# Performance work log

Hardware: AMD Instinct MI355X
Metric: run time of the kernel (lower is better)

The kernel has to match this reference:

```python
import jax, jax.numpy as jnp
import numpy as np
from jax import lax

T_DATA = 20000
E_NO = 2000
I_NO = 500
SUB_NO = 16
SYN_B = 3
HID = 256
T_SYN = 200
T_ENC = 80


def _causal_conv(x, kern):
    # x: [T, S] per-subunit drive; kern: [S, K] causal kernels (index = lag)
    S, K = kern.shape
    lhs = jnp.pad(x.T, ((0, 0), (K - 1, 0)))[None]        # [1, S, T+K-1]
    rhs = kern[:, ::-1][:, None, :]                        # flip then correlate == torch conv1d path
    out = lax.conv_general_dilated(lhs, rhs, (1,), 'VALID', feature_group_count=S)
    return out[0].T                                        # [T, S]


def setup_inputs() -> dict:
    key = jax.random.key(0)
    ks = jax.random.split(key, 16)
    V_in = jax.random.normal(ks[0], (T_DATA,), jnp.float32) * 5.0 - 69.0
    S_e = jax.random.bernoulli(ks[1], 0.02, (T_DATA, E_NO)).astype(jnp.float32)
    S_i = jax.random.bernoulli(ks[2], 0.02, (T_DATA, I_NO)).astype(jnp.float32)
    # synapse -> subunit one-hot assignment matrices [sub_no, n_syn]
    C_syn_e = jax.nn.one_hot(jax.random.randint(ks[3], (E_NO,), 0, SUB_NO), SUB_NO, dtype=jnp.float32).T
    C_syn_i = jax.nn.one_hot(jax.random.randint(ks[4], (I_NO,), 0, SUB_NO), SUB_NO, dtype=jnp.float32).T
    # parameters, initialized exactly as in __init__
    K_syn = jnp.stack([jnp.full((SUB_NO, SYN_B), 0.04),
                       jnp.full((SUB_NO, SYN_B), -0.02),
                       jnp.full((SUB_NO, SYN_B), 0.02)], axis=-1)          # [sub, B, 3]
    tau_syn = jnp.tile((jnp.arange(SYN_B, dtype=jnp.float32) + 1.6)[:, None], (1, 3))  # [B, 3]
    delta_syn = jnp.full((SUB_NO, 2), 2.0, jnp.float32)
    enc_bias = jnp.zeros((SUB_NO - 1,), jnp.float32)
    W_in = 2 * T_ENC - 1

    def lin(k, fan_out, fan_in):
        kw, kb = jax.random.split(k)
        s = 1.0 / np.sqrt(fan_in)
        return (jax.random.uniform(kw, (fan_out, fan_in), jnp.float32, -s, s),
                jax.random.uniform(kb, (fan_out,), jnp.float32, -s, s))

    W1, b1 = lin(ks[5], HID, W_in)
    W2, b2 = lin(ks[6], HID, HID)
    W3, b3 = lin(ks[7], HID, HID)
    W4, b4 = lin(ks[8], SUB_NO - 1, HID)
    a1 = jnp.float32(0.25)
    a2 = jnp.float32(0.25)
    a3 = jnp.float32(0.25)
    return dict(V_in=V_in, S_e=S_e, S_i=S_i, C_syn_e=C_syn_e, C_syn_i=C_syn_i,
                K_syn=K_syn, tau_syn=tau_syn, delta_syn=delta_syn, enc_bias=enc_bias,
                W1=W1, b1=b1, a1=a1, W2=W2, b2=b2, a2=a2, W3=W3, b3=b3, a3=a3,
                W4=W4, b4=b4)


def reference(V_in, S_e, S_i, C_syn_e, C_syn_i, K_syn, tau_syn, delta_syn, enc_bias,
              W1, b1, a1, W2, b2, a2, W3, b3, a3, W4, b4):
    T = V_in.shape[0]
    # ---- spike_convolve, fully vectorized over (subunit, basis) ----
    t = jnp.arange(T_SYN, dtype=V_in.dtype)                 # [T_syn]
    d = jnp.exp(delta_syn)                                   # [sub, 2]
    te = jnp.maximum(t[None, :] - d[:, 0:1], 0.0)            # [sub, T_syn]
    ti = jnp.maximum(t[None, :] - d[:, 1:2], 0.0)
    tau = jnp.exp(tau_syn)                                   # [B, 3]
    tte = te[:, None, :] / tau[None, :, 0, None]             # [sub, B, T_syn]
    tti = ti[:, None, :] / tau[None, :, 1, None]
    ker_e = jnp.einsum('sbt,sb->st', tte * jnp.exp(-tte), K_syn[:, :, 0])
    ker_i = jnp.einsum('sbt,sb->st', tti * jnp.exp(-tti), K_syn[:, :, 1])
    in_e = S_e @ C_syn_e.T                                   # [T, sub]
    in_i = S_i @ C_syn_i.T
    S_conv = _causal_conv(in_e, ker_e) + _causal_conv(in_i, ker_i)   # [T, sub]
    # ---- encode: batched sliding-window MLP (replaces per-timestep loop) ----
    W = 2 * T_ENC - 1
    Vpad = jnp.zeros((T + W,), V_in.dtype).at[T_ENC - 1:T_ENC - 1 + T].set(V_in)
    idx = jnp.arange(T)[:, None] + jnp.arange(W)[None, :]    # [T, W]
    win = Vpad[idx]                                          # [T, W]
    prelu = lambda x, a: jnp.where(x >= 0, x, a * x)
    h = prelu(win @ W1.T + b1, a1)
    h = prelu(h @ W2.T + b2, a2)
    h = prelu(h @ W3.T + b3, a3)
    nn_out = h @ W4.T + b4                                   # [T, sub-1]
    return jax.nn.sigmoid(nn_out + S_conv[:, 1:] + enc_bias)
```

## Files before the change

kernel.cpp:

```cpp
#include <hip/hip_runtime.h>
#include <cstdint>
#include <cstddef>

#define T_DATA 20000
#define E_NO 2000
#define I_NO 500
#define SUB_NO 16
#define HID 256
#define T_SYN 200
#define T_ENC 80
#define W_IN 159

typedef __attribute__((ext_vector_type(8))) __bf16 bf16x8;
typedef __attribute__((ext_vector_type(8))) short short8;
typedef __attribute__((ext_vector_type(4))) float floatx4;
typedef __attribute__((ext_vector_type(4))) unsigned int uint4v;
typedef __attribute__((ext_vector_type(2))) unsigned int uint2v;

__device__ __forceinline__ float bf2f(unsigned short u) {
    union { unsigned int i; float f; } v; v.i = ((unsigned int)u) << 16; return v.f;
}
__device__ __forceinline__ unsigned short f2bf(float f) {
    union { float f; unsigned int i; } v; v.f = f;
    unsigned int r = v.i + 0x7FFFu + ((v.i >> 16) & 1u);
    return (unsigned short)(r >> 16);
}
__device__ __forceinline__ float inload(const void* p, int i, int isbf) {
    return isbf ? bf2f(((const unsigned short*)p)[i]) : ((const float*)p)[i];
}

__device__ __forceinline__ int detect_bf(const void* Se, int* sfl) {
    if (threadIdx.x == 0) *sfl = 0;
    __syncthreads();
    const unsigned int* w = (const unsigned int*)Se;
    int la = 0;
    #pragma unroll
    for (int i = 0; i < 4; i++)
        la |= (w[i * 256 + threadIdx.x] & 0xFFFFu) ? 1 : 0;
    if (la) atomicOr(sfl, 1);
    __syncthreads();
    return *sfl;
}

#define OFF_KERE   16u
#define OFF_KERI   12816u
#define OFF_W1H    25616u
#define OFF_W1L    107536u
#define OFF_W2H    189456u
#define OFF_W2L    320528u
#define OFF_W3H    451600u
#define OFF_W3L    582672u
#define OFF_W4H    713744u
#define OFF_W4L    721424u
#define OFF_INE    729104u
#define OFF_INI    1049104u

__device__ __forceinline__ void acc_slot(unsigned int b, unsigned int sh,
                                         unsigned long long& lo, unsigned long long& hi) {
    unsigned int up = sh >> 6;
    unsigned int s6 = sh & 63;
    lo += (unsigned long long)(b & (up ^ 1u)) << s6;
    hi += (unsigned long long)(b & up) << s6;
}

#define SPIKE_BLOCKS 1250
#define SETUP_ITEMS  182272
#define SETUP_BLOCKS 712

__global__ void __launch_bounds__(256) k_front(
        const void* Se, const void* Si, const void* Ce, const void* Ci,
        const void* Ksyn, const void* tau_syn, const void* dly,
        const void* W1, const void* W2, const void* W3, const void* W4,
        float* ker_e, float* ker_i,
        unsigned short* W1h, unsigned short* W1l,
        unsigned short* W2h, unsigned short* W2l,
        unsigned short* W3h, unsigned short* W3l,
        unsigned short* W4h, unsigned short* W4l,
        unsigned char* in_e, unsigned char* in_i) {
    __shared__ int sfl;
    __shared__ __align__(8) unsigned char she[E_NO];
    __shared__ __align__(8) unsigned char shi[I_NO];
    int tid = threadIdx.x;

    if (blockIdx.x < SPIKE_BLOCKS) {
        if (tid == 0) sfl = 0;
        __syncthreads();
        {
            const unsigned int* w = (const unsigned int*)Se;
            int la = 0;
            #pragma unroll
            for (int i = 0; i < 4; i++)
                la |= (w[i * 256 + tid] & 0xFFFFu) ? 1 : 0;
            if (la) atomicOr(&sfl, 1);
        }
        __syncthreads();
        int f = sfl;
        for (int e = tid; e < E_NO; e += 256) {
            int a = 0;
            for (int s = 0; s < 16; s++) if (inload(Ce, s * E_NO + e, f) > 0.5f) a = s;
            she[e] = (unsigned char)(a * 8);
        }
        for (int e = tid; e < I_NO; e += 256) {
            int a = 0;
            for (int s = 0; s < 16; s++) if (inload(Ci, s * I_NO + e, f) > 0.5f) a = s;
            shi[e] = (unsigned char)(a * 8);
        }
        __syncthreads();
        int lane = tid & 63, wave = tid >> 6;
        #pragma unroll
        for (int j = 0; j < 4; j++) {
            int t = blockIdx.x * 16 + wave * 4 + j;
            unsigned long long e0 = 0, e1 = 0, i0 = 0, i1 = 0;
            if (f) {
                const uint4v* re = (const uint4v*)((const unsigned short*)Se + (size_t)t * E_NO);
                #pragma unroll
                for (int it = 0; it < 4; it++) {
                    int c = it * 64 + lane;
                    if (c < 250) {
                        uint4v v = re[c];
                        unsigned long long q = *(const unsigned long long*)&she[c * 8];
                        #pragma unroll
                        for (int w = 0; w < 4; w++) {
                            unsigned int x = v[w];
                            acc_slot((x >> 7) & 1u,  (unsigned int)(q >> (16 * w)) & 0xFFu, e0, e1);
                            acc_slot((x >> 23) & 1u, (unsigned int)(q >> (16 * w + 8)) & 0xFFu, e0, e1);
                        }
                    }
                }
                const uint2v* ri = (const uint2v*)((const unsigned short*)Si + (size_t)t * I_NO);
                #pragma unroll
                for (int it = 0; it < 2; it++) {
                    int c = it * 64 + lane;
                    if (c < 125) {
                        uint2v v = ri[c];
                        unsigned int q = *(const unsigned int*)&shi[c * 4];
                        #pragma unroll
                        for (int w = 0; w < 2; w++) {
                            unsigned int x = v[w];
                            acc_slot((x >> 7) & 1u,  (q >> (16 * w)) & 0xFFu, i0, i1);
                            acc_slot((x >> 23) & 1u, (q >> (16 * w + 8)) & 0xFFu, i0, i1);
                        }
                    }
                }
            } else {
                const uint4v* re = (const uint4v*)((const float*)Se + (size_t)t * E_NO);
                #pragma unroll
                for (int it = 0; it < 8; it++) {
                    int c = it * 64 + lane;
                    if (c < 500) {
                        uint4v v = re[c];
                        unsigned int q = *(const unsigned int*)&she[c * 4];
                        #pragma unroll
                        for (int w = 0; w < 4; w++)
                            acc_slot((v[w] >> 23) & 1u, (q >> (8 * w)) & 0xFFu, e0, e1);
                    }
                }
                const uint2v* ri = (const uint2v*)((const float*)Si + (size_t)t * I_NO);
                #pragma unroll
                for (int it = 0; it < 4; it++) {
                    int c = it * 64 + lane;
                    if (c < 250) {
                        uint2v v = ri[c];
                        unsigned int q = *(const unsigned short*)&shi[c * 2];
                        #pragma unroll
                        for (int w = 0; w < 2; w++)
                            acc_slot((v[w] >> 23) & 1u, (q >> (8 * w)) & 0xFFu, i0, i1);
                    }
                }
            }
            for (int off = 32; off; off >>= 1) {
                e0 += __shfl_xor(e0, off);
                e1 += __shfl_xor(e1, off);
                i0 += __shfl_xor(i0, off);
                i1 += __shfl_xor(i1, off);
            }
            if (lane < 16) {
                unsigned long long a = (lane < 8) ? e0 : e1;
                in_e[(size_t)t * 16 + lane] = (unsigned char)((a >> ((lane & 7) * 8)) & 0xFF);
            } else if (lane < 32) {
                int s = lane - 16;
                unsigned long long a = (s < 8) ? i0 : i1;
                in_i[(size_t)t * 16 + s] = (unsigned char)((a >> ((s & 7) * 8)) & 0xFF);
            }
        }
    } else {
        int f = detect_bf(Se, &sfl);
        int id = (blockIdx.x - SPIKE_BLOCKS) * 256 + tid;
        if (id < 6400) {
            int c = id < 3200 ? 0 : 1;
            int q = id - c * 3200;
            int s = q / 200, j = q - s * 200;
            float d = expf(inload(dly, s * 2 + c, f));
            float tt = fmaxf((float)j - d, 0.0f);
            float acc = 0.f;
            #pragma unroll
            for (int b = 0; b < 3; b++) {
                float tau = expf(inload(tau_syn, b * 3 + c, f));
                float x = tt / tau;
                acc += x * expf(-x) * inload(Ksyn, (s * 3 + b) * 3 + c, f);
            }
            (c == 0 ? ker_e : ker_i)[s * 200 + j] = acc;
        } else if (id < 47360) {
            int q = id - 6400;
            int n = q / 160, k = q - n * 160;
            float v = (k < W_IN) ? inload(W1, n * W_IN + k, f) : 0.f;
            unsigned short hi = f2bf(v);
            W1h[q] = hi;
            W1l[q] = f2bf(v - bf2f(hi));
        } else if (id < 112896) {
            int q = id - 47360;
            float v = inload(W2, q, f);
            unsigned short hi = f2bf(v);
            W2h[q] = hi;
            W2l[q] = f2bf(v - bf2f(hi));
        } else if (id < 178432) {
            int q = id - 112896;
            float v = inload(W3, q, f);
            unsigned short hi = f2bf(v);
            W3h[q] = hi;
            W3l[q] = f2bf(v - bf2f(hi));
        } else if (id < 182272) {
            int q = id - 178432;
            float v = inload(W4, q, f);
            unsigned short hi = f2bf(v);
            W4h[q] = hi;
            W4l[q] = f2bf(v - bf2f(hi));
        }
    }
}

template<bool BF>
__device__ __forceinline__ void mlp_body(
    const void* V,
    const unsigned short* W1h, const unsigned short* W1l, const void* b1, const void* a1p,
    const unsigned short* W2h, const unsigned short* W2l, const void* b2, const void* a2p,
    const unsigned short* W3h, const unsigned short* W3l, const void* b3, const void* a3p,
    const unsigned short* W4h, const unsigned short* W4l, const void* b4,
    const void* encb, const float* sc, void* out,
    unsigned short* Ahi, unsigned short* Alo)
{
    int tid = threadIdx.x;
    int lane = tid & 63, wave = tid >> 6;
    int lm = lane & 15, quad = lane >> 4;
    int t0 = blockIdx.x * 64;

    auto ld = [&](const void* p, int i) -> float {
        return BF ? bf2f(((const unsigned short*)p)[i]) : ((const float*)p)[i];
    };

    for (int idx = tid; idx < 64 * 160; idx += 256) {
        int m = idx / 160, k = idx - m * 160;
        int tg = t0 + m + k - (T_ENC - 1);
        float v = 0.f;
        if (k < W_IN && tg >= 0 && tg < T_DATA) v = ld(V, tg);
        unsigned short hi = f2bf(v);
        int col = (((k >> 3) ^ (m & 31)) << 3) | (k & 7);
        Ahi[m * 256 + col] = hi;
        if (!BF) Alo[m * 256 + col] = f2bf(v - bf2f(hi));
    }
    __syncthreads();

    floatx4 acc[4][4];
    auto aoff = [&](int mt, int ks) {
        int arow = mt * 16 + lm;
        return arow * 256 + ((((ks << 2) | quad) ^ (arow & 31)) << 3);
    };

    auto epi = [&](const void* bias, float alpha) {
        __syncthreads();
        #pragma unroll
        for (int mt = 0; mt < 4; mt++) {
            #pragma unroll
            for (int nt = 0; nt < 4; nt++) {
                int cn = wave * 64 + nt * 16 + lm;
                float bb = ld(bias, cn);
                #pragma unroll
                for (int j = 0; j < 4; j++) {
                    int row = mt * 16 + quad * 4 + j;
                    float h = acc[mt][nt][j] + bb;
                    h = (h >= 0.f) ? h : alpha * h;
                    unsigned short hi = f2bf(h);
                    int col = (((cn >> 3) ^ (row & 31)) << 3) | (cn & 7);
                    Ahi[row * 256 + col] = hi;
                    if (!BF) Alo[row * 256 + col] = f2bf(h - bf2f(hi));
                }
            }
        }
        __syncthreads();
    };

    floatx4 z = {0.f, 0.f, 0.f, 0.f};
    {
        #pragma unroll
        for (int mt = 0; mt < 4; mt++)
            #pragma unroll
            for (int nt = 0; nt < 4; nt++) acc[mt][nt] = z;
        if (BF) {
            bf16x8 Bh[5][4];
            #pragma unroll
            for (int ks = 0; ks < 5; ks++)
                #pragma unroll
                for (int nt = 0; nt < 4; nt++)
                    Bh[ks][nt] = *(const bf16x8*)(W1h + (size_t)(wave * 64 + nt * 16 + lm) * 160 + ks * 32 + quad * 8);
            #pragma unroll
            for (int ks = 0; ks < 5; ks++) {
                bf16x8 a[4];
                #pragma unroll
                for (int mt = 0; mt < 4; mt++) a[mt] = *(const bf16x8*)&Ahi[aoff(mt, ks)];
                #pragma unroll
                for (int nt = 0; nt < 4; nt++)
                    #pragma unroll
                    for (int mt = 0; mt < 4; mt++)
                        acc[mt][nt] = __builtin_amdgcn_mfma_f32_16x16x32_bf16(a[mt], Bh[ks][nt], acc[mt][nt], 0, 0, 0);
            }
        } else {
            for (int ks = 0; ks < 5; ks++) {
                bf16x8 ah[4], al[4];
                #pragma unroll
                for (int mt = 0; mt < 4; mt++) {
                    ah[mt] = *(const bf16x8*)&Ahi[aoff(mt, ks)];
                    al[mt] = *(const bf16x8*)&Alo[aoff(mt, ks)];
                }
                #pragma unroll
                for (int nt = 0; nt < 4; nt++) {
                    size_t bo = (size_t)(wave * 64 + nt * 16 + lm) * 160 + ks * 32 + quad * 8;
                    bf16x8 bh = *(const bf16x8*)(W1h + bo);
                    bf16x8 bl = *(const bf16x8*)(W1l + bo);
                    #pragma unroll
                    for (int mt = 0; mt < 4; mt++) {
                        acc[mt][nt] = __builtin_amdgcn_mfma_f32_16x16x32_bf16(ah[mt], bh, acc[mt][nt], 0, 0, 0);
                        acc[mt][nt] = __builtin_amdgcn_mfma_f32_16x16x32_bf16(al[mt], bh, acc[mt][nt], 0, 0, 0);
                        acc[mt][nt] = __builtin_amdgcn_mfma_f32_16x16x32_bf16(ah[mt], bl, acc[mt][nt], 0, 0, 0);
                    }
                }
            }
        }
        epi(b1, ld(a1p, 0));
    }
    const unsigned short* Whs[2] = {W2h, W3h};
    const unsigned short* Wls[2] = {W2l, W3l};
    const void* bs[2] = {b2, b3};
    const void* as_[2] = {a2p, a3p};
    for (int l = 0; l < 2; l++) {
        #pragma unroll
        for (int mt = 0; mt < 4; mt++)
            #pragma unroll
            for (int nt = 0; nt < 4; nt++) acc[mt][nt] = z;
        const unsigned short* Wh = Whs[l];
        const unsigned short* Wl = Wls[l];
        if (BF) {
            bf16x8 Bh[8][4];
            #pragma unroll
            for (int ks = 0; ks < 8; ks++)
                #pragma unroll
                for (int nt = 0; nt < 4; nt++)
                    Bh[ks][nt] = *(const bf16x8*)(Wh + (size_t)(wave * 64 + nt * 16 + lm) * 256 + ks * 32 + quad * 8);
            #pragma unroll
            for (int ks = 0; ks < 8; ks++) {
                bf16x8 a[4];
                #pragma unroll
                for (int mt = 0; mt < 4; mt++) a[mt] = *(const bf16x8*)&Ahi[aoff(mt, ks)];
                #pragma unroll
                for (int nt = 0; nt < 4; nt++)
                    #pragma unroll
                    for (int mt = 0; mt < 4; mt++)
                        acc[mt][nt] = __builtin_amdgcn_mfma_f32_16x16x32_bf16(a[mt], Bh[ks][nt], acc[mt][nt], 0, 0, 0);
            }
        } else {
            for (int ks = 0; ks < 8; ks++) {
                bf16x8 ah[4], al[4];
                #pragma unroll
                for (int mt = 0; mt < 4; mt++) {
                    ah[mt] = *(const bf16x8*)&Ahi[aoff(mt, ks)];
                    al[mt] = *(const bf16x8*)&Alo[aoff(mt, ks)];
                }
                #pragma unroll
                for (int nt = 0; nt < 4; nt++) {
                    size_t bo = (size_t)(wave * 64 + nt * 16 + lm) * 256 + ks * 32 + quad * 8;
                    bf16x8 bh = *(const bf16x8*)(Wh + bo);
                    bf16x8 bl = *(const bf16x8*)(Wl + bo);
                    #pragma unroll
                    for (int mt = 0; mt < 4; mt++) {
                        acc[mt][nt] = __builtin_amdgcn_mfma_f32_16x16x32_bf16(ah[mt], bh, acc[mt][nt], 0, 0, 0);
                        acc[mt][nt] = __builtin_amdgcn_mfma_f32_16x16x32_bf16(al[mt], bh, acc[mt][nt], 0, 0, 0);
                        acc[mt][nt] = __builtin_amdgcn_mfma_f32_16x16x32_bf16(ah[mt], bl, acc[mt][nt], 0, 0, 0);
                    }
                }
            }
        }
        epi(bs[l], ld(as_[l], 0));
    }
    {
        int mt = wave;
        short8 z8 = {0, 0, 0, 0, 0, 0, 0, 0};
        bf16x8 bz = __builtin_bit_cast(bf16x8, z8);
        floatx4 a4 = z;
        #pragma unroll
        for (int ks = 0; ks < 8; ks++) {
            bf16x8 ah = *(const bf16x8*)&Ahi[aoff(mt, ks)];
            bf16x8 bh = bz;
            if (lm < 15)
                bh = *(const bf16x8*)(W4h + (size_t)lm * 256 + ks * 32 + quad * 8);
            a4 = __builtin_amdgcn_mfma_f32_16x16x32_bf16(ah, bh, a4, 0, 0, 0);
            if (!BF) {
                bf16x8 al = *(const bf16x8*)&Alo[aoff(mt, ks)];
                bf16x8 bl = bz;
                if (lm < 15)
                    bl = *(const bf16x8*)(W4l + (size_t)lm * 256 + ks * 32 + quad * 8);
                a4 = __builtin_amdgcn_mfma_f32_16x16x32_bf16(al, bh, a4, 0, 0, 0);
                a4 = __builtin_amdgcn_mfma_f32_16x16x32_bf16(ah, bl, a4, 0, 0, 0);
            }
        }
        if (lm < 15) {
            float bb = ld(b4, lm) + ld(encb, lm);
            #pragma unroll
            for (int j = 0; j < 4; j++) {
                int row = mt * 16 + quad * 4 + j;
                int t = t0 + row;
                if (t < T_DATA) {
                    float x = a4[j] + bb + sc[row * 16 + lm + 1];
                    x = fminf(fmaxf(x, -40.f), 40.f);
                    float sg = 1.f / (1.f + expf(-x));
                    if (BF) ((unsigned short*)out)[(size_t)t * 15 + lm] = f2bf(sg);
                    else    ((float*)out)[(size_t)t * 15 + lm] = sg;
                }
            }
        }
    }
}

__global__ void __launch_bounds__(256, 2) k_back(
    const void* Se, const void* V,
    const unsigned char* in_e, const unsigned char* in_i,
    const float* ker_e, const float* ker_i,
    const unsigned short* W1h, const unsigned short* W1l, const void* b1, const void* a1p,
    const unsigned short* W2h, const unsigned short* W2l, const void* b2, const void* a2p,
    const unsigned short* W3h, const unsigned short* W3l, const void* b3, const void* a3p,
    const unsigned short* W4h, const unsigned short* W4l, const void* b4,
    const void* encb, void* out) {
    __shared__ __align__(16) char smem[65536];
    __shared__ __align__(16) float sc[64 * 16];
    __shared__ int sfl;
    int f = detect_bf(Se, &sfl);
    int tid = threadIdx.x;
    int t0 = blockIdx.x * 64;

    {
        float* se = (float*)smem;
        float* si = se + 263 * 17;
        float* ke = si + 263 * 17;
        float* ki = ke + 16 * 201;
        for (int idx = tid; idx < 263 * 4; idx += 256) {
            int r = idx >> 2, wi = idx & 3;
            int t = t0 - 199 + r;
            unsigned int ve = 0, vi = 0;
            if (t >= 0 && t < T_DATA) {
                ve = ((const unsigned int*)in_e)[t * 4 + wi];
                vi = ((const unsigned int*)in_i)[t * 4 + wi];
            }
            #pragma unroll
            for (int b = 0; b < 4; b++) {
                se[r * 17 + wi * 4 + b] = (float)((ve >> (8 * b)) & 0xFF);
                si[r * 17 + wi * 4 + b] = (float)((vi >> (8 * b)) & 0xFF);
            }
        }
        for (int idx = tid; idx < 3200; idx += 256) {
            int s = idx / 200, j = idx - s * 200;
            ke[s * 201 + j] = ker_e[idx];
            ki[s * 201 + j] = ker_i[idx];
        }
        __syncthreads();
        int s = tid & 15, g4 = (tid >> 4) * 4;
        float a0 = 0.f, a1 = 0.f, a2 = 0.f, a3 = 0.f;
        float w0 = se[(g4 + 199) * 17 + s], w1 = se[(g4 + 200) * 17 + s];
        float w2 = se[(g4 + 201) * 17 + s], w3 = se[(g4 + 202) * 17 + s];
        float x0 = si[(g4 + 199) * 17 + s], x1 = si[(g4 + 200) * 17 + s];
        float x2 = si[(g4 + 201) * 17 + s], x3 = si[(g4 + 202) * 17 + s];
        #pragma unroll 4
        for (int j = 0; j < 200; j++) {
            float kej = ke[s * 201 + j];
            float kij = ki[s * 201 + j];
            a0 += w0 * kej + x0 * kij;
            a1 += w1 * kej + x1 * kij;
            a2 += w2 * kej + x2 * kij;
            a3 += w3 * kej + x3 * kij;
            int lr = g4 + 198 - j; lr = lr < 0 ? 0 : lr;
            float nw = se[lr * 17 + s], nx = si[lr * 17 + s];
            w3 = w2; w2 = w1; w1 = w0; w0 = nw;
            x3 = x2; x2 = x1; x1 = x0; x0 = nx;
        }
        sc[(g4 + 0) * 16 + s] = a0;
        sc[(g4 + 1) * 16 + s] = a1;
        sc[(g4 + 2) * 16 + s] = a2;
        sc[(g4 + 3) * 16 + s] = a3;
        __syncthreads();
    }

    unsigned short* Ahi = (unsigned short*)smem;
    unsigned short* Alo = Ahi + 64 * 256;
    if (f)
        mlp_body<true>(V, W1h, W1l, b1, a1p, W2h, W2l, b2, a2p, W3h, W3l, b3, a3p,
                       W4h, W4l, b4, encb, sc, out, Ahi, Alo);
    else
        mlp_body<false>(V, W1h, W1l, b1, a1p, W2h, W2l, b2, a2p, W3h, W3l, b3, a3p,
                        W4h, W4l, b4, encb, sc, out, Ahi, Alo);
}

extern "C" void kernel_launch(void* const* d_in, const int* in_sizes, int n_in,
                              void* d_out, int out_size, void* d_ws, size_t ws_size,
                              hipStream_t stream) {
    const void* V    = d_in[0];
    const void* Se   = d_in[1];
    const void* Si   = d_in[2];
    const void* Ce   = d_in[3];
    const void* Ci   = d_in[4];
    const void* Ksyn = d_in[5];
    const void* tau  = d_in[6];
    const void* dly  = d_in[7];
    const void* encb = d_in[8];
    const void* W1   = d_in[9];
    const void* b1   = d_in[10];
    const void* a1   = d_in[11];
    const void* W2   = d_in[12];
    const void* b2   = d_in[13];
    const void* a2   = d_in[14];
    const void* W3   = d_in[15];
    const void* b3   = d_in[16];
    const void* a3   = d_in[17];
    const void* W4   = d_in[18];
    const void* b4   = d_in[19];

    char* w = (char*)d_ws;
    float* ker_e = (float*)(w + OFF_KERE);
    float* ker_i = (float*)(w + OFF_KERI);
    unsigned short* W1h = (unsigned short*)(w + OFF_W1H);
    unsigned short* W1l = (unsigned short*)(w + OFF_W1L);
    unsigned short* W2h = (unsigned short*)(w + OFF_W2H);
    unsigned short* W2l = (unsigned short*)(w + OFF_W2L);
    unsigned short* W3h = (unsigned short*)(w + OFF_W3H);
    unsigned short* W3l = (unsigned short*)(w + OFF_W3L);
    unsigned short* W4h = (unsigned short*)(w + OFF_W4H);
    unsigned short* W4l = (unsigned short*)(w + OFF_W4L);
    unsigned char* in_e = (unsigned char*)(w + OFF_INE);
    unsigned char* in_i = (unsigned char*)(w + OFF_INI);

    k_front<<<SPIKE_BLOCKS + SETUP_BLOCKS, 256, 0, stream>>>(
        Se, Si, Ce, Ci, Ksyn, tau, dly, W1, W2, W3, W4,
        ker_e, ker_i, W1h, W1l, W2h, W2l, W3h, W3l, W4h, W4l, in_e, in_i);
    k_back<<<313, 256, 0, stream>>>(
        Se, V, in_e, in_i, ker_e, ker_i,
        W1h, W1l, b1, a1, W2h, W2l, b2, a2, W3h, W3l, b3, a3,
        W4h, W4l, b4, encb, d_out);
}
```

Before: 381.4 us.

## Compute spike-to-subunit projection with bf16 MFMA instead of bit-packed scalar accumulation

Replaces the per-timestep scalar bit-extraction and packed 64-bit counter accumulation for S_e@C_e^T and S_i@C_i^T with 16x16x32 bf16 MFMA instructions. The one-hot matrices are loaded directly as MFMA A fragments, so the per-block shared-memory assignment table is no longer built. Each wave covers a K slice, and the partial sums are reduced through shared memory and rounded to bytes. Float inputs are truncated to bf16, which is exact for 0/1 values. Format detection now runs in all blocks.

```diff
diff --git a/kernel.cpp b/kernel.cpp
--- a/kernel.cpp
+++ b/kernel.cpp
@@ -55,17 +55,102 @@
 #define OFF_INE    729104u
 #define OFF_INI    1049104u
 
-__device__ __forceinline__ void acc_slot(unsigned int b, unsigned int sh,
-                                         unsigned long long& lo, unsigned long long& hi) {
-    unsigned int up = sh >> 6;
-    unsigned int s6 = sh & 63;
-    lo += (unsigned long long)(b & (up ^ 1u)) << s6;
-    hi += (unsigned long long)(b & up) << s6;
-}
-
 #define SPIKE_BLOCKS 1250
-#define SETUP_ITEMS  182272
 #define SETUP_BLOCKS 712
+
+__device__ __forceinline__ bf16x8 hi_pack(uint4v u0, uint4v u1) {
+    uint4v r;
+    r[0] = (u0[0] >> 16) | (u0[1] & 0xFFFF0000u);
+    r[1] = (u0[2] >> 16) | (u0[3] & 0xFFFF0000u);
+    r[2] = (u1[0] >> 16) | (u1[1] & 0xFFFF0000u);
+    r[3] = (u1[2] >> 16) | (u1[3] & 0xFFFF0000u);
+    return __builtin_bit_cast(bf16x8, r);
+}
+template<bool BF>
+__device__ __forceinline__ bf16x8 ldfrag(const void* p, size_t idx) {
+    if (BF) return *(const bf16x8*)((const unsigned short*)p + idx);
+    const float* f = (const float*)p + idx;
+    return hi_pack(*(const uint4v*)f, *(const uint4v*)(f + 4));
+}
+template<bool BF>
+__device__ __forceinline__ bf16x8 ldfrag4(const void* p, size_t idx) {
+    uint4v r = {0u, 0u, 0u, 0u};
+    if (BF) {
+        uint2v u = *(const uint2v*)((const unsigned short*)p + idx);
+        r[0] = u[0]; r[1] = u[1];
+    } else {
+        uint4v u = *(const uint4v*)((const float*)p + idx);
+        r[0] = (u[0] >> 16) | (u[1] & 0xFFFF0000u);
+        r[1] = (u[2] >> 16) | (u[3] & 0xFFFF0000u);
+    }
+    return __builtin_bit_cast(bf16x8, r);
+}
+
+template<bool BF>
+__device__ __forceinline__ void spike_gemm(const void* Se, const void* Si,
+        const void* Ce, const void* Ci,
+        unsigned char* in_e, unsigned char* in_i, float* red) {
+    int tid = threadIdx.x;
+    int lane = tid & 63, wave = tid >> 6;
+    int lm = lane & 15, quad = lane >> 4;
+    int t0 = blockIdx.x * 16;
+    size_t teb = (size_t)(t0 + lm) * E_NO;
+    size_t tib = (size_t)(t0 + lm) * I_NO;
+    floatx4 ae = {0.f, 0.f, 0.f, 0.f}, ai = {0.f, 0.f, 0.f, 0.f};
+    short8 zs = {0, 0, 0, 0, 0, 0, 0, 0};
+    bf16x8 bz = __builtin_bit_cast(bf16x8, zs);
+
+    #pragma unroll
+    for (int q = 0; q < 16; q++) {
+        int kg = wave * 16 + q;
+        int k0 = kg * 32 + quad * 8;
+        bf16x8 a = bz, b = bz;
+        if (kg < 63 && (kg < 62 || quad < 2)) {
+            a = ldfrag<BF>(Ce, (size_t)lm * E_NO + k0);
+            b = ldfrag<BF>(Se, teb + k0);
+        }
+        ae = __builtin_amdgcn_mfma_f32_16x16x32_bf16(a, b, ae, 0, 0, 0);
+    }
+    #pragma unroll
+    for (int q = 0; q < 4; q++) {
+        int kg = wave * 4 + q;
+        int k0 = kg * 32 + quad * 8;
+        bf16x8 a = bz, b = bz;
+        if (kg < 15 || quad < 2) {
+            a = ldfrag<BF>(Ci, (size_t)lm * I_NO + k0);
+            b = ldfrag<BF>(Si, tib + k0);
+        } else if (quad == 2) {
+            a = ldfrag4<BF>(Ci, (size_t)lm * I_NO + k0);
+            b = ldfrag4<BF>(Si, tib + k0);
+        }
+        ai = __builtin_amdgcn_mfma_f32_16x16x32_bf16(a, b, ai, 0, 0, 0);
+    }
+    float* re = red;
+    float* ri = red + 1024;
+    #pragma unroll
+    for (int j = 0; j < 4; j++) {
+        re[wave * 256 + (quad * 4 + j) * 16 + lm] = ae[j];
+        ri[wave * 256 + (quad * 4 + j) * 16 + lm] = ai[j];
+    }
+    __syncthreads();
+    if (tid < 64) {
+        int t = tid >> 2, qd = tid & 3;
+        unsigned pe = 0, pi = 0;
+        #pragma unroll
+        for (int j = 0; j < 4; j++) {
+            float se_ = 0.f, si_ = 0.f;
+            #pragma unroll
+            for (int w = 0; w < 4; w++) {
+                se_ += re[w * 256 + (qd * 4 + j) * 16 + t];
+                si_ += ri[w * 256 + (qd * 4 + j) * 16 + t];
+            }
+            pe |= ((unsigned)(se_ + 0.5f) & 0xFFu) << (8 * j);
+            pi |= ((unsigned)(si_ + 0.5f) & 0xFFu) << (8 * j);
+        }
+        ((unsigned*)in_e)[(t0 + t) * 4 + qd] = pe;
+        ((unsigned*)in_i)[(t0 + t) * 4 + qd] = pi;
+    }
+}
 
 __global__ void __launch_bounds__(256) k_front(
         const void* Se, const void* Si, const void* Ce, const void* Ci,
@@ -78,113 +163,14 @@
         unsigned short* W4h, unsigned short* W4l,
         unsigned char* in_e, unsigned char* in_i) {
     __shared__ int sfl;
-    __shared__ __align__(8) unsigned char she[E_NO];
-    __shared__ __align__(8) unsigned char shi[I_NO];
+    __shared__ __align__(16) float red[2048];
+    int f = detect_bf(Se, &sfl);
     int tid = threadIdx.x;
 
     if (blockIdx.x < SPIKE_BLOCKS) {
-        if (tid == 0) sfl = 0;
-        __syncthreads();
-        {
-            const unsigned int* w = (const unsigned int*)Se;
-            int la = 0;
-            #pragma unroll
-            for (int i = 0; i < 4; i++)
-                la |= (w[i * 256 + tid] & 0xFFFFu) ? 1 : 0;
-            if (la) atomicOr(&sfl, 1);
-        }
-        __syncthreads();
-        int f = sfl;
-        for (int e = tid; e < E_NO; e += 256) {
-            int a = 0;
-            for (int s = 0; s < 16; s++) if (inload(Ce, s * E_NO + e, f) > 0.5f) a = s;
-            she[e] = (unsigned char)(a * 8);
-        }
-        for (int e = tid; e < I_NO; e += 256) {
-            int a = 0;
-            for (int s = 0; s < 16; s++) if (inload(Ci, s * I_NO + e, f) > 0.5f) a = s;
-            shi[e] = (unsigned char)(a * 8);
-        }
-        __syncthreads();
-        int lane = tid & 63, wave = tid >> 6;
-        #pragma unroll
-        for (int j = 0; j < 4; j++) {
-            int t = blockIdx.x * 16 + wave * 4 + j;
-            unsigned long long e0 = 0, e1 = 0, i0 = 0, i1 = 0;
-            if (f) {
-                const uint4v* re = (const uint4v*)((const unsigned short*)Se + (size_t)t * E_NO);
-                #pragma unroll
-                for (int it = 0; it < 4; it++) {
-                    int c = it * 64 + lane;
-                    if (c < 250) {
-                        uint4v v = re[c];
-                        unsigned long long q = *(const unsigned long long*)&she[c * 8];
-                        #pragma unroll
-                        for (int w = 0; w < 4; w++) {
-                            unsigned int x = v[w];
-                            acc_slot((x >> 7) & 1u,  (unsigned int)(q >> (16 * w)) & 0xFFu, e0, e1);
-                            acc_slot((x >> 23) & 1u, (unsigned int)(q >> (16 * w + 8)) & 0xFFu, e0, e1);
-                        }
-                    }
-                }
-                const uint2v* ri = (const uint2v*)((const unsigned short*)Si + (size_t)t * I_NO);
-                #pragma unroll
-                for (int it = 0; it < 2; it++) {
-                    int c = it * 64 + lane;
-                    if (c < 125) {
-                        uint2v v = ri[c];
-                        unsigned int q = *(const unsigned int*)&shi[c * 4];
-                        #pragma unroll
-                        for (int w = 0; w < 2; w++) {
-                            unsigned int x = v[w];
-                            acc_slot((x >> 7) & 1u,  (q >> (16 * w)) & 0xFFu, i0, i1);
-                            acc_slot((x >> 23) & 1u, (q >> (16 * w + 8)) & 0xFFu, i0, i1);
-                        }
-                    }
-                }
-            } else {
-                const uint4v* re = (const uint4v*)((const float*)Se + (size_t)t * E_NO);
-                #pragma unroll
-                for (int it = 0; it < 8; it++) {
-                    int c = it * 64 + lane;
-                    if (c < 500) {
-                        uint4v v = re[c];
-                        unsigned int q = *(const unsigned int*)&she[c * 4];
-                        #pragma unroll
-                        for (int w = 0; w < 4; w++)
-                            acc_slot((v[w] >> 23) & 1u, (q >> (8 * w)) & 0xFFu, e0, e1);
-                    }
-                }
-                const uint2v* ri = (const uint2v*)((const float*)Si + (size_t)t * I_NO);
-                #pragma unroll
-                for (int it = 0; it < 4; it++) {
-                    int c = it * 64 + lane;
-                    if (c < 250) {
-                        uint2v v = ri[c];
-                        unsigned int q = *(const unsigned short*)&shi[c * 2];
-                        #pragma unroll
-                        for (int w = 0; w < 2; w++)
-                            acc_slot((v[w] >> 23) & 1u, (q >> (8 * w)) & 0xFFu, i0, i1);
-                    }
-                }
-            }
-            for (int off = 32; off; off >>= 1) {
-                e0 += __shfl_xor(e0, off);
-                e1 += __shfl_xor(e1, off);
-                i0 += __shfl_xor(i0, off);
-                i1 += __shfl_xor(i1, off);
-            }
-            if (lane < 16) {
-                unsigned long long a = (lane < 8) ? e0 : e1;
-                in_e[(size_t)t * 16 + lane] = (unsigned char)((a >> ((lane & 7) * 8)) & 0xFF);
-            } else if (lane < 32) {
-                int s = lane - 16;
-                unsigned long long a = (s < 8) ? i0 : i1;
-                in_i[(size_t)t * 16 + s] = (unsigned char)((a >> ((s & 7) * 8)) & 0xFF);
-            }
-        }
+        if (f) spike_gemm<true>(Se, Si, Ce, Ci, in_e, in_i, red);
+        else   spike_gemm<false>(Se, Si, Ce, Ci, in_e, in_i, red);
     } else {
-        int f = detect_bf(Se, &sfl);
         int id = (blockIdx.x - SPIKE_BLOCKS) * 256 + tid;
         if (id < 6400) {
             int c = id < 3200 ? 0 : 1;
```

After: 377.9 us. About the same (-0.9%).
